# Kernel optimization log

Hardware: AMD Instinct MI355X
Metric: run time of the kernel (lower is better)

## Reference

```python
import jax, jax.numpy as jnp
import numpy as np

REPR_IN = (16, 16, 8)
REPR_OUT = (32, 16, 8)
NUM_BASIS = 16
MAX_RADIUS = 2.0
GAMMA = 16.0  # radial basis sharpness

def _dim(repr_):
    return sum(m * (2 * l + 1) for l, m in enumerate(repr_))

DIM_IN = _dim(REPR_IN)          # 104
SIZE_OUT = _dim(REPR_OUT)       # 120
NUM_GATES = sum(REPR_OUT[1:])   # 24
DIM_OUT = SIZE_OUT + NUM_GATES  # 144 (conv emits gates too)


def setup_inputs() -> dict:
    key = jax.random.key(0)
    k1, k2, k3, k4 = jax.random.split(key, 4)
    B, N, M = 4, 1024, 1024
    features = jax.random.normal(k1, (B, DIM_IN, M), jnp.float32)
    difference_matrix = jax.random.normal(k2, (B, N, M, 3), jnp.float32)
    relative_mask = jax.random.uniform(k3, (B, N, M), jnp.float32)
    W = jax.random.normal(k4, (NUM_BASIS, DIM_OUT, DIM_IN), jnp.float32) / np.sqrt(NUM_BASIS * DIM_IN)
    return {"features": features, "difference_matrix": difference_matrix,
            "relative_mask": relative_mask, "W": W}


def _radial_basis(diff):
    # diff: [B, N, M, 3] -> phi: [B, N, M, K]
    r = jnp.sqrt(jnp.sum(diff * diff, axis=-1) + 1e-12)
    centers = jnp.linspace(0.0, MAX_RADIUS, NUM_BASIS, dtype=diff.dtype)
    return jnp.exp(-GAMMA * jnp.square(r[..., None] - centers))


def reference(features, difference_matrix, relative_mask, W):
    # SE3PointConvolution: per-pair kernel K[b,n,m] = sum_k phi_k(|r_nm|) W[k]
    # masked by relative_mask; out[b,o,n] = sum_m K[b,n,m,o,i] feat[b,i,m].
    # Fused so the [B,N,M,144,104] kernel is never materialized.
    phi = _radial_basis(difference_matrix) * relative_mask[..., None]  # [B,N,M,K]
    tmp = jnp.einsum('bnmk,bim->bnki', phi, features)                  # [B,N,K,DIM_IN]
    y = jnp.einsum('bnki,koi->bon', tmp, W)                            # [B,DIM_OUT,N]

    B, _, N = y.shape
    # scalar (l=0) activation, bias=False
    outs = [jax.nn.relu(y[:, :REPR_OUT[0]])]
    # gates: last NUM_GATES channels, sigmoid
    g = jax.nn.sigmoid(y[:, SIZE_OUT:])
    begin_y, begin_g = REPR_OUT[0], 0
    for l, mul in enumerate(REPR_OUT):
        if l == 0 or mul == 0:
            continue
        d = 2 * l + 1
        fy = y[:, begin_y:begin_y + mul * d].reshape(B, mul, d, N)
        fg = g[:, begin_g:begin_g + mul].reshape(B, mul, 1, N)
        outs.append((fy * fg).reshape(B, mul * d, N))
        begin_y += mul * d
        begin_g += mul
    return jnp.concatenate(outs, axis=1)  # [B, SIZE_OUT, N]
```

## Files before the change

### kernel.cpp

```cpp
#include <hip/hip_runtime.h>


typedef __attribute__((ext_vector_type(4))) float f32x4;
typedef __attribute__((ext_vector_type(8))) short s16x8;

#define DI 104
#define DO 144
#define TTST 1688
#define YST 9

#define W_ELEMS 239616
#define F_ELEMS 425984

#define OFF_PHI0 0
#define OFF_PHI1 16384
#define OFF_FEAT0 32768
#define OFF_FEAT1 47104
#define OFF_Y 61440
#define SMEM_TOTAL (61440 + 144*9*4)

__device__ __forceinline__ float fexp2(float x) {
#if __has_builtin(__builtin_amdgcn_exp2f)
    return __builtin_amdgcn_exp2f(x);
#else
    return exp2f(x);
#endif
}
__device__ __forceinline__ float flog2(float x) {
#if __has_builtin(__builtin_amdgcn_logf)
    return __builtin_amdgcn_logf(x);
#else
    return log2f(x);
#endif
}
__device__ __forceinline__ float fsqrt_(float x) {
#if __has_builtin(__builtin_amdgcn_sqrtf)
    return __builtin_amdgcn_sqrtf(x);
#else
    return sqrtf(x);
#endif
}
__device__ __forceinline__ float frcp_(float x) {
#if __has_builtin(__builtin_amdgcn_rcpf)
    return __builtin_amdgcn_rcpf(x);
#else
    return 1.0f / x;
#endif
}
__device__ __forceinline__ unsigned int pkbf(float lo, float hi) {
    unsigned int a = __builtin_bit_cast(unsigned int, lo) + 0x8000u;
    unsigned int b = __builtin_bit_cast(unsigned int, hi) + 0x8000u;
    return __builtin_amdgcn_perm(b, a, 0x07060302u);
}
__device__ __forceinline__ unsigned short f2b(float f) {
    return (unsigned short)((__builtin_bit_cast(unsigned int, f) + 0x8000u) >> 16);
}

__global__ __launch_bounds__(256, 8)
void cvt_kernel(const float* __restrict__ feat_g, const float* __restrict__ W_g,
                unsigned short* __restrict__ ws)
{
    int gid = blockIdx.x * 256 + threadIdx.x;
    const float* src;
    unsigned short* dst;
    if (gid < W_ELEMS/8) {
        src = W_g + gid*8;  dst = ws + gid*8;
    } else {
        int g2 = gid - W_ELEMS/8;
        src = feat_g + g2*8; dst = ws + W_ELEMS + g2*8;
    }
    f32x4 a = *(const f32x4*)src;
    f32x4 b = *(const f32x4*)(src + 4);
    unsigned int o[4] = { pkbf(a[0],a[1]), pkbf(a[2],a[3]), pkbf(b[0],b[1]), pkbf(b[2],b[3]) };
    *(f32x4*)dst = *(f32x4*)o;
}

#define LOAD_DM(M0)                                                    \
    do {                                                               \
        const float* dp_ = diff_g + (dmrow + (M0) + pml)*3;            \
        dx0 = dp_[0]; dy0 = dp_[1]; dz0 = dp_[2];                      \
        dx1 = dp_[3]; dy1 = dp_[4]; dz1 = dp_[5];                      \
        const float* mp_ = mask_g + dmrow + (M0) + pml;                \
        mk0 = mp_[0]; mk1 = mp_[1];                                    \
    } while (0)

#define LOAD_FEAT(M0)                                                          \
    do {                                                                       \
        fr0 = *(const s16x8*)(featbf + fbase + ((size_t)fi0 << 10) + (M0) + (fj << 3)); \
        if (t < 320)                                                           \
            fr1 = *(const s16x8*)(featbf + fbase + ((size_t)fi1 << 10) + (M0) + (fj << 3)); \
    } while (0)

#define COMPUTE_PHI()                                                  \
    do {                                                               \
        float r0_ = fsqrt_(fmaf(dx0,dx0, fmaf(dy0,dy0, fmaf(dz0,dz0, 1e-12f)))); \
        float r1_ = fsqrt_(fmaf(dx1,dx1, fmaf(dy1,dy1, fmaf(dz1,dz1, 1e-12f)))); \
        float t0_ = r0_ - K0OFF, t1_ = r1_ - K0OFF;                    \
        float E0_ = fmaf(CEXP*t0_, t0_, flog2(mk0));                   \
        float E1_ = fmaf(CEXP*t1_, t1_, flog2(mk1));                   \
        float s0_ = fmaf(A1, r0_, S0B);                                \
        float s1_ = fmaf(A1, r1_, S0B);                                \
        _Pragma("unroll")                                              \
        for (int j_ = 0; j_ < 8; ++j_) {                               \
            pk[j_] = pkbf(fexp2(E0_), fexp2(E1_));                     \
            E0_ += s0_; s0_ += V2;                                     \
            E1_ += s1_; s1_ += V2;                                     \
        }                                                              \
    } while (0)

#define WRITE_PHI(BUF)                                                 \
    do {                                                               \
        unsigned short* pw_ = (BUF) + (pn*16 + kh*8)*64 + pin;         \
        _Pragma("unroll")                                              \
        for (int j_ = 0; j_ < 8; ++j_)                                 \
            *(unsigned int*)(pw_ + j_*64 + ((pblk ^ j_) << 3)) = pk[j_]; \
    } while (0)

#define WRITE_FEAT(BUF)                                                \
    do {                                                               \
        *(s16x8*)((BUF) + fi0*64 + fjs) = fr0;                         \
        if (t < 320) *(s16x8*)((BUF) + fi1*64 + fjs) = fr1;            \
    } while (0)

#define GEMM1(PBUF, FBUF)                                              \
    do {                                                               \
        _Pragma("unroll")                                              \
        for (int kk_ = 0; kk_ < 2; ++kk_) {                            \
            const int mo_ = ((kk_*4 + q) ^ sw) << 3;                   \
            s16x8 a0_ = *(const s16x8*)((PBUF) + ((2*wr    )*16 + l15)*64 + mo_); \
            s16x8 a1_ = *(const s16x8*)((PBUF) + ((2*wr + 1)*16 + l15)*64 + mo_); \
            _Pragma("unroll")                                          \
            for (int cc_ = 0; cc_ < 4; ++cc_) {                        \
                if (ct0 + cc_ < 7) {                                   \
                    s16x8 bf_ = *(const s16x8*)((FBUF) + ((ct0+cc_)*16 + l15)*64 + mo_); \
                    acc[0][cc_] = __builtin_amdgcn_mfma_f32_16x16x32_bf16(a0_, bf_, acc[0][cc_], 0, 0, 0); \
                    acc[1][cc_] = __builtin_amdgcn_mfma_f32_16x16x32_bf16(a1_, bf_, acc[1][cc_], 0, 0, 0); \
                }                                                      \
            }                                                          \
        }                                                              \
    } while (0)

__global__ __launch_bounds__(512, 4)
void pgb_kernel(const unsigned short* __restrict__ ws,
                const float* __restrict__ diff_g,
                const float* __restrict__ mask_g,
                float* __restrict__ out_g)
{
    const unsigned short* Wbf    = ws;
    const unsigned short* featbf = ws + W_ELEMS;

    __shared__ __align__(16) unsigned char smem[SMEM_TOTAL];
    unsigned short* Tt   = (unsigned short*)smem;
    float*          ylds = (float*)(smem + OFF_Y);
    unsigned short* phi0b  = (unsigned short*)(smem + OFF_PHI0);
    unsigned short* phi1b  = (unsigned short*)(smem + OFF_PHI1);
    unsigned short* feat0b = (unsigned short*)(smem + OFF_FEAT0);
    unsigned short* feat1b = (unsigned short*)(smem + OFF_FEAT1);

    const int t    = threadIdx.x;
    const int b    = blockIdx.x >> 7;
    const int n0   = (blockIdx.x & 127) << 3;
    const int wave = t >> 6;
    const int lane = t & 63;
    const int l15  = lane & 15;
    const int q    = lane >> 4;
    const int wr   = wave >> 1;
    const int ct0  = (wave & 1) << 2;
    const int sw   = l15 & 7;

    if (t < 256) {
        ((unsigned int*)(smem + OFF_FEAT0 + DI*128))[t] = 0u;
        ((unsigned int*)(smem + OFF_FEAT1 + DI*128))[t] = 0u;
    }

    f32x4 acc[2][4];
#pragma unroll
    for (int rr = 0; rr < 2; ++rr)
#pragma unroll
        for (int cc = 0; cc < 4; ++cc)
            acc[rr][cc] = (f32x4){0.f, 0.f, 0.f, 0.f};

    const int pn   = t >> 6;
    const int kh   = (t >> 5) & 1;
    const int pml  = (t & 31) << 1;
    const int pblk = (t & 31) >> 2;
    const int pin  = pml & 7;
    const float CEXP = -23.083120654223414f;
    const float A1   = 6.155498841126244f;
    const float V2   = -0.8207331788168325f;
    const float K0OFF = kh ? 1.0666666666666667f : 0.f;
    const float S0B   = kh ? -6.976232019943076f : -0.41036658940841624f;
    const size_t dmrow = (size_t)((b << 10) + n0 + pn) << 10;

    const int fi0 = t >> 3, fj = t & 7;
    const int fi1 = 64 + (t >> 3);
    const int fjs = (fj ^ (fi0 & 7)) << 3;
    const size_t fbase = (size_t)b * DI << 10;

    float dx0, dy0, dz0, dx1, dy1, dz1, mk0, mk1;
    s16x8 fr0 = {}, fr1 = {};
    unsigned int pk[8];

    LOAD_DM(0);
    LOAD_FEAT(0);
    COMPUTE_PHI();
    WRITE_PHI(phi0b);
    WRITE_FEAT(feat0b);
    LOAD_DM(64);
    LOAD_FEAT(64);

    for (int s = 0; s < 15; ++s) {
        unsigned short* rp = (s & 1) ? phi1b  : phi0b;
        unsigned short* rf = (s & 1) ? feat1b : feat0b;
        unsigned short* wp = (s & 1) ? phi0b  : phi1b;
        unsigned short* wf = (s & 1) ? feat0b : feat1b;
        __syncthreads();
        COMPUTE_PHI();
        WRITE_PHI(wp);
        WRITE_FEAT(wf);
        {
            const int mnext = (s < 14 ? (s + 2) : 15) * 64;
            LOAD_DM(mnext);
            LOAD_FEAT(mnext);
        }
        GEMM1(rp, rf);
    }
    __syncthreads();
    GEMM1(phi1b, feat1b);

    __syncthreads();

#pragma unroll
    for (int rr = 0; rr < 2; ++rr) {
        int nloc = 2*wr + rr;
#pragma unroll
        for (int cc = 0; cc < 4; ++cc) {
            int i = (ct0+cc)*16 + l15;
            if (ct0 + cc < 7 && i < DI) {
#pragma unroll
                for (int r = 0; r < 4; ++r)
                    Tt[nloc*TTST + (q*4+r)*DI + i] = f2b(acc[rr][cc][r]);
            }
        }
    }
    __syncthreads();

    f32x4 y0 = (f32x4){0.f,0.f,0.f,0.f}, y1 = (f32x4){0.f,0.f,0.f,0.f};
    const int o0 = wave*16 + l15;
    const int o1 = 128 + l15;
#pragma unroll 4
    for (int s3 = 0; s3 < 52; ++s3) {
        int a = s3*4 + q;
        int k = a / 13;
        int i = (a - k*13) << 3;
        s16x8 bf = *(const s16x8*)(Tt + (l15 & 7)*TTST + s3*32 + q*8);
        s16x8 af = *(const s16x8*)(Wbf + (size_t)(k*DO + o0)*DI + i);
        y0 = __builtin_amdgcn_mfma_f32_16x16x32_bf16(af, bf, y0, 0, 0, 0);
        if (wave == 0) {
            s16x8 ag = *(const s16x8*)(Wbf + (size_t)(k*DO + o1)*DI + i);
            y1 = __builtin_amdgcn_mfma_f32_16x16x32_bf16(ag, bf, y1, 0, 0, 0);
        }
    }
    if (l15 < 8) {
#pragma unroll
        for (int r = 0; r < 4; ++r)
            ylds[(wave*16 + q*4 + r)*YST + l15] = y0[r];
        if (wave == 0) {
#pragma unroll
            for (int r = 0; r < 4; ++r)
                ylds[(128 + q*4 + r)*YST + l15] = y1[r];
        }
    }
    __syncthreads();

    const float L2E = 1.4426950408889634f;
    for (int idx = t; idx < 120*8; idx += 512) {
        int o = idx >> 3, nn = idx & 7;
        float y = ylds[o*YST + nn];
        float v;
        if (o < 32) {
            v = fmaxf(y, 0.f);
        } else if (o < 80) {
            float g = ylds[(120 + (o-32)/3)*YST + nn];
            v = y * frcp_(1.f + fexp2(-g*L2E));
        } else {
            float g = ylds[(136 + (o-80)/5)*YST + nn];
            v = y * frcp_(1.f + fexp2(-g*L2E));
        }
        out_g[((size_t)(b*120 + o) << 10) + n0 + nn] = v;
    }
}

extern "C" void kernel_launch(void* const* d_in, const int* in_sizes, int n_in,
                              void* d_out, int out_size, void* d_ws, size_t ws_size,
                              hipStream_t stream) {
    const float* feat = (const float*)d_in[0];
    const float* diff = (const float*)d_in[1];
    const float* mask = (const float*)d_in[2];
    const float* W    = (const float*)d_in[3];
    float* out = (float*)d_out;
    unsigned short* ws = (unsigned short*)d_ws;
    (void)in_sizes; (void)n_in; (void)out_size; (void)ws_size;
    cvt_kernel<<<dim3((W_ELEMS + F_ELEMS)/8/256), dim3(256), 0, stream>>>(feat, W, ws);
    pgb_kernel<<<dim3(512), dim3(512), 0, stream>>>(ws, diff, mask, out);
}
```

Measured before the change: 141.1 us.

## Read feature GEMM operand directly from global memory instead of LDS staging

Drops the double-buffered LDS staging of bf16 features. The GEMM B operand is now loaded straight from global memory (through the caches) inside the MFMA loop, and the padded last tile is zero-filled in registers. This shrinks shared memory to 32 KB and raises the launch-bounds occupancy hint, aiming to cut LDS traffic and stores and to allow more resident blocks. In exchange the global load latency sits inside the inner loop with no prefetch, and the tighter launch bound may force register spills.

After: 247.5 us. +75.3%, slower.

```diff
diff --git a/kernel.cpp b/kernel.cpp
--- a/kernel.cpp
+++ b/kernel.cpp
@@ -14,10 +14,8 @@
 
 #define OFF_PHI0 0
 #define OFF_PHI1 16384
-#define OFF_FEAT0 32768
-#define OFF_FEAT1 47104
-#define OFF_Y 61440
-#define SMEM_TOTAL (61440 + 144*9*4)
+#define OFF_Y 27008
+#define SMEM_TOTAL 32768
 
 __device__ __forceinline__ float fexp2(float x) {
 #if __has_builtin(__builtin_amdgcn_exp2f)
@@ -82,13 +80,6 @@
         dx1 = dp_[3]; dy1 = dp_[4]; dz1 = dp_[5];                      \
         const float* mp_ = mask_g + dmrow + (M0) + pml;                \
         mk0 = mp_[0]; mk1 = mp_[1];                                    \
-    } while (0)
-
-#define LOAD_FEAT(M0)                                                          \
-    do {                                                                       \
-        fr0 = *(const s16x8*)(featbf + fbase + ((size_t)fi0 << 10) + (M0) + (fj << 3)); \
-        if (t < 320)                                                           \
-            fr1 = *(const s16x8*)(featbf + fbase + ((size_t)fi1 << 10) + (M0) + (fj << 3)); \
     } while (0)
 
 #define COMPUTE_PHI()                                                  \
@@ -116,13 +107,7 @@
             *(unsigned int*)(pw_ + j_*64 + ((pblk ^ j_) << 3)) = pk[j_]; \
     } while (0)
 
-#define WRITE_FEAT(BUF)                                                \
-    do {                                                               \
-        *(s16x8*)((BUF) + fi0*64 + fjs) = fr0;                         \
-        if (t < 320) *(s16x8*)((BUF) + fi1*64 + fjs) = fr1;            \
-    } while (0)
-
-#define GEMM1(PBUF, FBUF)                                              \
+#define GEMM1(PBUF, MB)                                                \
     do {                                                               \
         _Pragma("unroll")                                              \
         for (int kk_ = 0; kk_ < 2; ++kk_) {                            \
@@ -132,7 +117,14 @@
             _Pragma("unroll")                                          \
             for (int cc_ = 0; cc_ < 4; ++cc_) {                        \
                 if (ct0 + cc_ < 7) {                                   \
-                    s16x8 bf_ = *(const s16x8*)((FBUF) + ((ct0+cc_)*16 + l15)*64 + mo_); \
+                    s16x8 bf_;                                         \
+                    if (ct0 + cc_ == 6) {                              \
+                        bf_ = (s16x8){0,0,0,0,0,0,0,0};                \
+                        if (l15 < 8)                                   \
+                            bf_ = *(const s16x8*)(featbf + boff[cc_] + (MB) + kk_*32); \
+                    } else {                                           \
+                        bf_ = *(const s16x8*)(featbf + boff[cc_] + (MB) + kk_*32); \
+                    }                                                  \
                     acc[0][cc_] = __builtin_amdgcn_mfma_f32_16x16x32_bf16(a0_, bf_, acc[0][cc_], 0, 0, 0); \
                     acc[1][cc_] = __builtin_amdgcn_mfma_f32_16x16x32_bf16(a1_, bf_, acc[1][cc_], 0, 0, 0); \
                 }                                                      \
@@ -140,7 +132,7 @@
         }                                                              \
     } while (0)
 
-__global__ __launch_bounds__(512, 4)
+__global__ __launch_bounds__(512, 8)
 void pgb_kernel(const unsigned short* __restrict__ ws,
                 const float* __restrict__ diff_g,
                 const float* __restrict__ mask_g,
@@ -154,8 +146,6 @@
     float*          ylds = (float*)(smem + OFF_Y);
     unsigned short* phi0b  = (unsigned short*)(smem + OFF_PHI0);
     unsigned short* phi1b  = (unsigned short*)(smem + OFF_PHI1);
-    unsigned short* feat0b = (unsigned short*)(smem + OFF_FEAT0);
-    unsigned short* feat1b = (unsigned short*)(smem + OFF_FEAT1);
 
     const int t    = threadIdx.x;
     const int b    = blockIdx.x >> 7;
@@ -167,11 +157,6 @@
     const int wr   = wave >> 1;
     const int ct0  = (wave & 1) << 2;
     const int sw   = l15 & 7;
-
-    if (t < 256) {
-        ((unsigned int*)(smem + OFF_FEAT0 + DI*128))[t] = 0u;
-        ((unsigned int*)(smem + OFF_FEAT1 + DI*128))[t] = 0u;
-    }
 
     f32x4 acc[2][4];
 #pragma unroll
@@ -192,41 +177,35 @@
     const float S0B   = kh ? -6.976232019943076f : -0.41036658940841624f;
     const size_t dmrow = (size_t)((b << 10) + n0 + pn) << 10;
 
-    const int fi0 = t >> 3, fj = t & 7;
-    const int fi1 = 64 + (t >> 3);
-    const int fjs = (fj ^ (fi0 & 7)) << 3;
-    const size_t fbase = (size_t)b * DI << 10;
+    unsigned int boff[4];
+#pragma unroll
+    for (int cc = 0; cc < 4; ++cc)
+        boff[cc] = (unsigned int)(b * DI * 1024)
+                 + (unsigned int)(((ct0 + cc) * 16 + l15) * 1024)
+                 + (unsigned int)(q << 3);
 
     float dx0, dy0, dz0, dx1, dy1, dz1, mk0, mk1;
-    s16x8 fr0 = {}, fr1 = {};
     unsigned int pk[8];
 
     LOAD_DM(0);
-    LOAD_FEAT(0);
     COMPUTE_PHI();
     WRITE_PHI(phi0b);
-    WRITE_FEAT(feat0b);
     LOAD_DM(64);
-    LOAD_FEAT(64);
 
     for (int s = 0; s < 15; ++s) {
-        unsigned short* rp = (s & 1) ? phi1b  : phi0b;
-        unsigned short* rf = (s & 1) ? feat1b : feat0b;
-        unsigned short* wp = (s & 1) ? phi0b  : phi1b;
-        unsigned short* wf = (s & 1) ? feat0b : feat1b;
+        unsigned short* rp = (s & 1) ? phi1b : phi0b;
+        unsigned short* wp = (s & 1) ? phi0b : phi1b;
         __syncthreads();
         COMPUTE_PHI();
         WRITE_PHI(wp);
-        WRITE_FEAT(wf);
         {
             const int mnext = (s < 14 ? (s + 2) : 15) * 64;
             LOAD_DM(mnext);
-            LOAD_FEAT(mnext);
-        }
-        GEMM1(rp, rf);
-    }
-    __syncthreads();
-    GEMM1(phi1b, feat1b);
+        }
+        GEMM1(rp, s << 6);
+    }
+    __syncthreads();
+    GEMM1(phi1b, 15 << 6);
 
     __syncthreads();
 
```
